# Kernel tuning notes

Hardware: AMD Instinct MI355X
Metric: run time of the kernel (lower is better)

The kernel has to match this reference:

```python
import jax, jax.numpy as jnp
import numpy as np

LAM = 0.5          # lambda_ in DyGCN
GROUPS = 4
EPS_GN = 1e-5
EPS_LN = 1e-5


def _group_norm(y, w, b):
    # y: [B, Ch, N, T]; GroupNorm over (channels-in-group, N, T)
    B, Ch, N, T = y.shape
    yr = y.reshape(B, GROUPS, Ch // GROUPS, N, T)
    mu = yr.mean(axis=(2, 3, 4), keepdims=True)
    var = yr.var(axis=(2, 3, 4), keepdims=True)
    yn = ((yr - mu) * jax.lax.rsqrt(var + EPS_GN)).reshape(B, Ch, N, T)
    return yn * w[None, :, None, None] + b[None, :, None, None]


def _gtu(X, w, b, pw, pb, qw, qb):
    # grouped conv2d, kernel (1,k), stride 1, VALID; out channels = 2*H
    xc = jax.lax.conv_general_dilated(
        X, w, window_strides=(1, 1), padding='VALID',
        feature_group_count=GROUPS,
        dimension_numbers=('NCHW', 'OIHW', 'NCHW'))
    xc = xc + b[None, :, None, None]
    H = X.shape[1]
    xp = _group_norm(xc[:, :H], pw, pb)   # matches torch chunk(2, dim=1)
    xq = _group_norm(xc[:, H:], qw, qb)
    mish = xp * jnp.tanh(jax.nn.softplus(xp))   # Mish
    gate = jnp.clip(xq, 0.0, 1.0)               # Hardtanh(0,1)
    return mish * gate


def reference(x, static_adj, U1, U2, U3, be, Ve, W0, b0, masks, Ws, bs, Wd, bd,
              conv3_w, conv5_w, conv7_w, conv9_w, conv_b,
              gn_pw, gn_pb, gn_qw, gn_qb, fc_w, fc_b, res_w, res_b, ln_w, ln_b):
    B, N, C, T = x.shape
    # ---- Temporal attention ----
    lhs = jnp.einsum('btc,cn->btn', jnp.einsum('bnct,n->btc', x, U1), U2)  # [B,T,N]
    rhs = jnp.einsum('c,bnct->bnt', U3, x)                                 # [B,N,T]
    product = jnp.einsum('btn,bns->bts', lhs, rhs)                          # [B,T,T]
    E = jnp.einsum('ij,bjk->bik', Ve, jax.nn.sigmoid(product + be))
    At = jax.nn.softmax(E, axis=1)
    x_TAt = jnp.einsum('bmt,bts->bms', x.reshape(B, N * C, T), At).reshape(B, N, C, T)
    # ---- DyGCN, vectorized across T ----
    xt = jnp.moveaxis(x_TAt, -1, 1)                                        # [B,T,N,C]
    x0 = jnp.einsum('btnc,hc->btnh', xt, W0) + b0                          # shared linear
    enh = static_adj[None] * jax.nn.sigmoid(masks)                         # [T,N,N]
    s = jnp.einsum('tnm,btmc->btnc', enh, xt)
    static_out = jnp.einsum('btnc,thc->btnh', s, Ws) + bs[None, :, None, :]
    # dynamic branch (DynamicGCNLayer): data-dependent adjacency
    scores = jnp.einsum('btnc,btmc->btnm', xt, xt) / jnp.sqrt(jnp.float32(C))
    adj = jax.nn.softmax(scores, axis=-1)                                  # [B,T,N,N]
    d = jnp.einsum('btnm,btmc->btnc', adj, xt)
    dyn_out = jnp.einsum('btnc,thc->btnh', d, Wd) + bd[None, :, None, :]
    fused = (LAM - 0.025) * static_out + (1.0 - LAM - 0.025) * dyn_out + 0.05 * x0
    X = jnp.transpose(fused, (0, 3, 2, 1))                                 # [B,H,N,T]
    # ---- multi-scale gated temporal convs ----
    outs = [
        _gtu(X, conv3_w, conv_b[0], gn_pw[0], gn_pb[0], gn_qw[0], gn_qb[0]),
        _gtu(X, conv5_w, conv_b[1], gn_pw[1], gn_pb[1], gn_qw[1], gn_qb[1]),
        _gtu(X, conv7_w, conv_b[2], gn_pw[2], gn_pb[2], gn_qw[2], gn_qb[2]),
        _gtu(X, conv9_w, conv_b[3], gn_pw[3], gn_pb[3], gn_qw[3], gn_qb[3]),
    ]
    tc = jnp.concatenate(outs, axis=-1)                                    # [B,H,N,4T-20]
    tc = jnp.einsum('bhnk,ok->bhno', tc, fc_w) + fc_b                      # fcmy (dropout=eval no-op)
    tco = jax.nn.relu(tc)                                                  # [B,H,N,T]
    # ---- residual + LayerNorm ----
    residual = jnp.einsum('bnct,hc->bhnt', x, res_w) + res_b[None, :, None, None]
    y = jax.nn.relu(residual + tco)                                        # [B,H,N,T]
    yp = jnp.transpose(y, (0, 3, 2, 1))                                    # [B,T,N,H]
    mu = yp.mean(axis=-1, keepdims=True)
    var = yp.var(axis=-1, keepdims=True)
    yn = (yp - mu) * jax.lax.rsqrt(var + EPS_LN) * ln_w + ln_b
    return jnp.transpose(yn, (0, 2, 3, 1))                                 # [B,N,H,T]


def setup_inputs():
    key = jax.random.key(0)
    ks = jax.random.split(key, 32)
    B, N, C, T, H = 16, 512, 64, 12, 64
    w = 0.05
    A = jax.random.uniform(ks[0], (N, N), jnp.float32)
    A = A / A.sum(axis=-1, keepdims=True)  # row-normalized static adjacency
    return {
        'x': jax.random.normal(ks[1], (B, N, C, T), jnp.float32),
        'static_adj': A,
        'U1': jax.random.normal(ks[2], (N,), jnp.float32) * w,
        'U2': jax.random.normal(ks[3], (C, N), jnp.float32) * w,
        'U3': jax.random.normal(ks[4], (C,), jnp.float32) * w,
        'be': jax.random.normal(ks[5], (1, T, T), jnp.float32) * w,
        'Ve': jax.random.normal(ks[6], (T, T), jnp.float32) * w,
        'W0': jax.random.normal(ks[7], (H, C), jnp.float32) * w,
        'b0': jnp.zeros((H,), jnp.float32),
        'masks': jax.random.uniform(ks[8], (T, N, N), jnp.float32, 0.8, 1.2),
        'Ws': jax.random.normal(ks[9], (T, H, C), jnp.float32) * w,
        'bs': jnp.zeros((T, H), jnp.float32),
        'Wd': jax.random.normal(ks[10], (T, H, C), jnp.float32) * w,
        'bd': jnp.zeros((T, H), jnp.float32),
        'conv3_w': jax.random.normal(ks[11], (2 * H, H // 4, 1, 3), jnp.float32) * w,
        'conv5_w': jax.random.normal(ks[12], (2 * H, H // 4, 1, 5), jnp.float32) * w,
        'conv7_w': jax.random.normal(ks[13], (2 * H, H // 4, 1, 7), jnp.float32) * w,
        'conv9_w': jax.random.normal(ks[14], (2 * H, H // 4, 1, 9), jnp.float32) * w,
        'conv_b': jnp.zeros((4, 2 * H), jnp.float32),
        'gn_pw': jnp.ones((4, H), jnp.float32),
        'gn_pb': jnp.zeros((4, H), jnp.float32),
        'gn_qw': jnp.ones((4, H), jnp.float32),
        'gn_qb': jnp.zeros((4, H), jnp.float32),
        'fc_w': jax.random.normal(ks[15], (T, 4 * T - 20), jnp.float32) * w,
        'fc_b': jnp.zeros((T,), jnp.float32),
        'res_w': jax.random.normal(ks[16], (H, C), jnp.float32) * w,
        'res_b': jnp.zeros((H,), jnp.float32),
        'ln_w': jnp.ones((H,), jnp.float32),
        'ln_b': jnp.zeros((H,), jnp.float32),
    }
```

## Files before the change

### kernel.cpp

```cpp
#include <hip/hip_runtime.h>

constexpr int Bb = 16, Nn = 512, Cc = 64, Tt = 12, Hh = 64;
constexpr int NCT = Nn * Cc * Tt;
constexpr int CT  = Cc * Tt;

__global__ void k0_rest(const float* __restrict__ rw, float* __restrict__ resT) {
    int i = blockIdx.x * 256 + threadIdx.x;
    if (i < Hh * Cc) {
        int h = i >> 6, c = i & 63;
        resT[c * 64 + h] = rw[i];
    }
}

__global__ void k1a_tmp1(const float* __restrict__ x, const float* __restrict__ U1,
                         float* __restrict__ tmp1) {
    int blk = blockIdx.x;
    int b = blk / 12; int r = blk % 12;
    int ctb = r >> 2; int nch = r & 3;
    int ct = ctb * 256 + threadIdx.x;
    const float* xb = x + (size_t)b * NCT;
    float acc = 0.f;
    int n0 = nch * 128;
    for (int n = n0; n < n0 + 128; ++n)
        acc += xb[n * CT + ct] * U1[n];
    atomicAdd(&tmp1[b * CT + ct], acc);
}

__global__ void k1b_rhs(const float* __restrict__ x, const float* __restrict__ U3,
                        float* __restrict__ rhs) {
    int wid = blockIdx.x * 4 + (threadIdx.x >> 6);
    int b = wid >> 9; int n = wid & 511;
    int l = threadIdx.x & 63;
    const float4* x4 = (const float4*)(x + (size_t)(b * Nn + n) * CT);
    float4 a0 = x4[3 * l], a1 = x4[3 * l + 1], a2 = x4[3 * l + 2];
    float xv[12] = {a0.x,a0.y,a0.z,a0.w, a1.x,a1.y,a1.z,a1.w, a2.x,a2.y,a2.z,a2.w};
    float u = U3[l];
    float p[12];
    #pragma unroll
    for (int t = 0; t < 12; ++t) p[t] = u * xv[t];
    #pragma unroll
    for (int off = 1; off < 64; off <<= 1) {
        #pragma unroll
        for (int t = 0; t < 12; ++t) p[t] += __shfl_xor(p[t], off);
    }
    if (l == 0) {
        float* rp = rhs + (size_t)(b * Nn + n) * 12;
        *(float4*)(rp)     = make_float4(p[0], p[1], p[2], p[3]);
        *(float4*)(rp + 4) = make_float4(p[4], p[5], p[6], p[7]);
        *(float4*)(rp + 8) = make_float4(p[8], p[9], p[10], p[11]);
    }
}

__global__ void k1c_att(const float* __restrict__ tmp1, const float* __restrict__ rhs,
                        const float* __restrict__ U2, const float* __restrict__ be,
                        const float* __restrict__ Ve, float* __restrict__ At) {
    __shared__ float t1[CT];
    __shared__ float rh[Nn * Tt];
    __shared__ float lh[Tt * Nn];
    __shared__ float part[576];
    __shared__ float sp[144];
    __shared__ float Ee[144];
    int b = blockIdx.x, tid = threadIdx.x;
    for (int i = tid; i < CT; i += 256) t1[i] = tmp1[b * CT + i];
    for (int i = tid; i < Nn * Tt; i += 256) rh[i] = rhs[b * Nn * Tt + i];
    __syncthreads();
    for (int nn = tid; nn < Nn; nn += 256) {
        float l[Tt];
        #pragma unroll
        for (int t = 0; t < Tt; ++t) l[t] = 0.f;
        for (int c = 0; c < Cc; ++c) {
            float u2 = U2[c * Nn + nn];
            #pragma unroll
            for (int t = 0; t < Tt; ++t) l[t] += t1[c * Tt + t] * u2;
        }
        #pragma unroll
        for (int t = 0; t < Tt; ++t) lh[t * Nn + nn] = l[t];
    }
    __syncthreads();
    for (int task = tid; task < 576; task += 256) {
        int ts = task >> 2, ch = task & 3;
        int t = ts / 12, s2 = ts % 12;
        int n0 = ch * 128;
        float a = 0.f;
        for (int nn = n0; nn < n0 + 128; ++nn) a += lh[t * Nn + nn] * rh[nn * Tt + s2];
        part[task] = a;
    }
    __syncthreads();
    if (tid < 144) {
        float a = part[tid * 4] + part[tid * 4 + 1] + part[tid * 4 + 2] + part[tid * 4 + 3]
                + be[tid];
        sp[tid] = 1.f / (1.f + __expf(-a));
    }
    __syncthreads();
    if (tid < 144) {
        int i = tid / 12, k = tid % 12;
        float a = 0.f;
        #pragma unroll
        for (int j = 0; j < 12; ++j) a += Ve[i * 12 + j] * sp[j * 12 + k];
        Ee[tid] = a;
    }
    __syncthreads();
    if (tid < 12) {
        int k = tid;
        float mx = -1e30f;
        #pragma unroll
        for (int i = 0; i < 12; ++i) mx = fmaxf(mx, Ee[i * 12 + k]);
        float su = 0.f; float ex[12];
        #pragma unroll
        for (int i = 0; i < 12; ++i) { ex[i] = __expf(Ee[i * 12 + k] - mx); su += ex[i]; }
        float inv = 1.f / su;
        #pragma unroll
        for (int i = 0; i < 12; ++i) At[b * 144 + i * 12 + k] = ex[i] * inv;
    }
}

__global__ void k2_xtt(const float* __restrict__ x, const float* __restrict__ At,
                       float* __restrict__ xtT) {
    int idx = blockIdx.x * 256 + threadIdx.x;
    int n = idx & 511; int c = (idx >> 9) & 63; int b = idx >> 15;
    const float* xr = x + (size_t)((b * Nn + n) * Cc + c) * Tt;
    float xv[Tt];
    {
        const float4* x4 = (const float4*)xr;
        float4 a0 = x4[0], a1 = x4[1], a2 = x4[2];
        xv[0]=a0.x; xv[1]=a0.y; xv[2]=a0.z; xv[3]=a0.w;
        xv[4]=a1.x; xv[5]=a1.y; xv[6]=a1.z; xv[7]=a1.w;
        xv[8]=a2.x; xv[9]=a2.y; xv[10]=a2.z; xv[11]=a2.w;
    }
    const float* Ab = At + b * 144;
    for (int t = 0; t < Tt; ++t) {
        float a = 0.f;
        #pragma unroll
        for (int u = 0; u < Tt; ++u) a += xv[u] * Ab[u * 12 + t];
        xtT[((size_t)(b * Tt + t) * Cc + c) * Nn + n] = a;
    }
}

__global__ void k2b_enh(const float* __restrict__ adj, const float* __restrict__ masks,
                        float* __restrict__ enhT) {
    __shared__ float tile[32][33];
    int blk = blockIdx.x;
    int t = blk >> 8; int r = blk & 255;
    int n0 = (r >> 4) * 32; int m0 = (r & 15) * 32;
    int tx = threadIdx.x & 31; int ty = threadIdx.x >> 5;
    #pragma unroll
    for (int i = 0; i < 4; ++i) {
        int nl = ty + 8 * i;
        float a  = adj[(n0 + nl) * Nn + m0 + tx];
        float mk = masks[t * Nn * Nn + (n0 + nl) * Nn + m0 + tx];
        tile[nl][tx] = a / (1.f + __expf(-mk));
    }
    __syncthreads();
    #pragma unroll
    for (int i = 0; i < 4; ++i) {
        int ml = ty + 8 * i;
        enhT[(size_t)(t * Nn + m0 + ml) * Nn + n0 + tx] = tile[tx][ml];
    }
}

__global__ __launch_bounds__(256, 3) void k3_gcn(
    const float* __restrict__ xtT, const float* __restrict__ enhT,
    const float* __restrict__ W0, const float* __restrict__ b0,
    const float* __restrict__ Ws, const float* __restrict__ bs,
    const float* __restrict__ Wd, const float* __restrict__ bd,
    float* __restrict__ F) {
    __shared__ float xs[64][64];
    int blk = blockIdx.x;
    int seg = blk & 7; int t = (blk >> 3) % Tt; int b = blk / (Tt * 8);
    int tid = threadIdx.x;
    int lane = tid & 63;
    int w = tid >> 6;
    int cg = lane >> 4;
    int r = lane & 15;
    int n = seg * 64 + w * 16 + r;
    int c0 = cg * 16;
    const float* xb = xtT + (size_t)(b * Tt + t) * Cc * Nn;
    float row[16], accd[16], accs[16];
    #pragma unroll
    for (int j = 0; j < 16; ++j) row[j] = xb[(c0 + j) * Nn + n];
    #pragma unroll
    for (int j = 0; j < 16; ++j) { accd[j] = 0.f; accs[j] = 0.f; }
    float sumexp = 0.f;
    const float* ehT = enhT + (size_t)t * Nn * Nn + n;
    for (int m0 = 0; m0 < Nn; m0 += 64) {
        __syncthreads();
        #pragma unroll
        for (int i = 0; i < 4; ++i) {
            int f = i * 256 + tid;
            int c = f >> 4; int mi = (f & 15) * 4;
            *(float4*)&xs[c][mi] = *(const float4*)(xb + c * Nn + m0 + mi);
        }
        __syncthreads();
        #pragma unroll 1
        for (int m4 = 0; m4 < 64; m4 += 4) {
            float e0 = ehT[(m0 + m4 + 0) * Nn];
            float e1 = ehT[(m0 + m4 + 1) * Nn];
            float e2 = ehT[(m0 + m4 + 2) * Nn];
            float e3 = ehT[(m0 + m4 + 3) * Nn];
            float4 v[16];
            #pragma unroll
            for (int j = 0; j < 16; ++j) v[j] = *(const float4*)&xs[c0 + j][m4];
            float s0 = 0.f, s1 = 0.f, s2 = 0.f, s3 = 0.f;
            #pragma unroll
            for (int j = 0; j < 16; ++j) {
                float rj = row[j];
                s0 += rj * v[j].x; s1 += rj * v[j].y;
                s2 += rj * v[j].z; s3 += rj * v[j].w;
            }
            s0 += __shfl_xor(s0, 16); s0 += __shfl_xor(s0, 32);
            s1 += __shfl_xor(s1, 16); s1 += __shfl_xor(s1, 32);
            s2 += __shfl_xor(s2, 16); s2 += __shfl_xor(s2, 32);
            s3 += __shfl_xor(s3, 16); s3 += __shfl_xor(s3, 32);
            float p0 = __expf(s0 * 0.125f), p1 = __expf(s1 * 0.125f);
            float p2 = __expf(s2 * 0.125f), p3 = __expf(s3 * 0.125f);
            sumexp += (p0 + p1) + (p2 + p3);
            #pragma unroll
            for (int j = 0; j < 16; ++j) {
                accd[j] += p0 * v[j].x + p1 * v[j].y + p2 * v[j].z + p3 * v[j].w;
                accs[j] += e0 * v[j].x + e1 * v[j].y + e2 * v[j].z + e3 * v[j].w;
            }
        }
    }
    float invd = 0.475f / sumexp;
    #pragma unroll
    for (int j = 0; j < 16; ++j) {
        accd[j] *= invd; accs[j] *= 0.475f; row[j] *= 0.05f;
    }
    const float* Wst = Ws + t * Hh * Cc;
    const float* Wdt = Wd + t * Hh * Cc;
    float* Fp = F + ((size_t)(b * Tt + t) * Nn + n) * Hh;
    for (int hb = 0; hb < 16; ++hb) {
        float oo[4];
        #pragma unroll
        for (int k = 0; k < 4; ++k) {
            int h = hb * 4 + k;
            const float4* w04 = (const float4*)(W0 + h * Cc + c0);
            const float4* ws4 = (const float4*)(Wst + h * Cc + c0);
            const float4* wd4 = (const float4*)(Wdt + h * Cc + c0);
            float a = 0.f;
            #pragma unroll
            for (int jj = 0; jj < 4; ++jj) {
                float4 wv = w04[jj], sv = ws4[jj], dv = wd4[jj];
                a += row[jj*4+0]*wv.x + row[jj*4+1]*wv.y + row[jj*4+2]*wv.z + row[jj*4+3]*wv.w;
                a += accs[jj*4+0]*sv.x + accs[jj*4+1]*sv.y + accs[jj*4+2]*sv.z + accs[jj*4+3]*sv.w;
                a += accd[jj*4+0]*dv.x + accd[jj*4+1]*dv.y + accd[jj*4+2]*dv.z + accd[jj*4+3]*dv.w;
            }
            a += __shfl_xor(a, 16);
            a += __shfl_xor(a, 32);
            oo[k] = a + 0.05f * b0[h] + 0.475f * (bs[t * Hh + h] + bd[t * Hh + h]);
        }
        if ((hb >> 2) == cg)
            *(float4*)(Fp + hb * 4) = make_float4(oo[0], oo[1], oo[2], oo[3]);
    }
}

__global__ __launch_bounds__(512) void k4_conv(
                        const float* __restrict__ F,
                        const float* __restrict__ w3, const float* __restrict__ w5,
                        const float* __restrict__ w7, const float* __restrict__ w9,
                        const float* __restrict__ cb,
                        float* __restrict__ xc, float* __restrict__ stats) {
    __shared__ float fl[4 * Tt * Hh];
    __shared__ float sstat[64];
    int blk = blockIdx.x;
    int b = blk >> 7; int n0 = (blk & 127) * 4;
    int tid = threadIdx.x;
    if (tid < 64) sstat[tid] = 0.f;
    for (int i = tid; i < 3072; i += 512) {
        int t = i >> 8; int r = i & 255;
        fl[i] = F[(size_t)(b * Tt + t) * Nn * Hh + n0 * Hh + r];
    }
    __syncthreads();
    int nl = tid >> 7; int co = tid & 127;
    int g = co >> 5;
    float a3[10], a5[8], a7[6], a9[4];
    {
        float c3 = cb[co], c5 = cb[128 + co], c7 = cb[256 + co], c9 = cb[384 + co];
        #pragma unroll
        for (int j = 0; j < 10; ++j) a3[j] = c3;
        #pragma unroll
        for (int j = 0; j < 8; ++j) a5[j] = c5;
        #pragma unroll
        for (int j = 0; j < 6; ++j) a7[j] = c7;
        #pragma unroll
        for (int j = 0; j < 4; ++j) a9[j] = c9;
    }
    for (int ci = 0; ci < 16; ++ci) {
        int cig = g * 16 + ci;
        float xr[12];
        #pragma unroll
        for (int tt = 0; tt < 12; ++tt) xr[tt] = fl[tt * 256 + nl * 64 + cig];
        const float* p3 = w3 + (co * 16 + ci) * 3;
        #pragma unroll
        for (int dt = 0; dt < 3; ++dt) {
            float wv = p3[dt];
            #pragma unroll
            for (int j = 0; j < 10; ++j) a3[j] += xr[j + dt] * wv;
        }
        const float* p5 = w5 + (co * 16 + ci) * 5;
        #pragma unroll
        for (int dt = 0; dt < 5; ++dt) {
            float wv = p5[dt];
            #pragma unroll
            for (int j = 0; j < 8; ++j) a5[j] += xr[j + dt] * wv;
        }
        const float* p7 = w7 + (co * 16 + ci) * 7;
        #pragma unroll
        for (int dt = 0; dt < 7; ++dt) {
            float wv = p7[dt];
            #pragma unroll
            for (int j = 0; j < 6; ++j) a7[j] += xr[j + dt] * wv;
        }
        const float* p9 = w9 + (co * 16 + ci) * 9;
        #pragma unroll
        for (int dt = 0; dt < 9; ++dt) {
            float wv = p9[dt];
            #pragma unroll
            for (int j = 0; j < 4; ++j) a9[j] += xr[j + dt] * wv;
        }
    }
    int pg = (co < 64) ? (co >> 4) : 4 + ((co - 64) >> 4);
    float* xcw = xc + ((size_t)(b * Nn + n0 + nl) * 128 + co) * 28;
    float su, sq;
    su = 0.f; sq = 0.f;
    #pragma unroll
    for (int j = 0; j < 10; ++j) { float v = a3[j]; xcw[j] = v; su += v; sq += v * v; }
    #pragma unroll
    for (int off = 1; off < 16; off <<= 1) { su += __shfl_xor(su, off); sq += __shfl_xor(sq, off); }
    if ((tid & 15) == 0) { atomicAdd(&sstat[(0 * 8 + pg) * 2], su); atomicAdd(&sstat[(0 * 8 + pg) * 2 + 1], sq); }
    su = 0.f; sq = 0.f;
    #pragma unroll
    for (int j = 0; j < 8; ++j) { float v = a5[j]; xcw[10 + j] = v; su += v; sq += v * v; }
    #pragma unroll
    for (int off = 1; off < 16; off <<= 1) { su += __shfl_xor(su, off); sq += __shfl_xor(sq, off); }
    if ((tid & 15) == 0) { atomicAdd(&sstat[(1 * 8 + pg) * 2], su); atomicAdd(&sstat[(1 * 8 + pg) * 2 + 1], sq); }
    su = 0.f; sq = 0.f;
    #pragma unroll
    for (int j = 0; j < 6; ++j) { float v = a7[j]; xcw[18 + j] = v; su += v; sq += v * v; }
    #pragma unroll
    for (int off = 1; off < 16; off <<= 1) { su += __shfl_xor(su, off); sq += __shfl_xor(sq, off); }
    if ((tid & 15) == 0) { atomicAdd(&sstat[(2 * 8 + pg) * 2], su); atomicAdd(&sstat[(2 * 8 + pg) * 2 + 1], sq); }
    su = 0.f; sq = 0.f;
    #pragma unroll
    for (int j = 0; j < 4; ++j) { float v = a9[j]; xcw[24 + j] = v; su += v; sq += v * v; }
    #pragma unroll
    for (int off = 1; off < 16; off <<= 1) { su += __shfl_xor(su, off); sq += __shfl_xor(sq, off); }
    if ((tid & 15) == 0) { atomicAdd(&sstat[(3 * 8 + pg) * 2], su); atomicAdd(&sstat[(3 * 8 + pg) * 2 + 1], sq); }
    __syncthreads();
    if (tid < 64) {
        int s = tid >> 4; int pgq = (tid >> 1) & 7; int st = tid & 1;
        atomicAdd(&stats[((s * Bb + b) * 8 + pgq) * 2 + st], sstat[(s * 8 + pgq) * 2 + st]);
    }
}

__global__ __launch_bounds__(256) void k5_final(
                         const float* __restrict__ xc, const float* __restrict__ stats,
                         const float* __restrict__ x,
                         const float* __restrict__ gpw, const float* __restrict__ gpb,
                         const float* __restrict__ gqw, const float* __restrict__ gqb,
                         const float* __restrict__ fcw, const float* __restrict__ fcb,
                         const float* __restrict__ resT, const float* __restrict__ rb,
                         const float* __restrict__ lnw, const float* __restrict__ lnb,
                         float* __restrict__ out) {
    int blk = blockIdx.x;
    int b = blk >> 7; int n = (blk & 127) * 4 + (threadIdx.x >> 6);
    int h = threadIdx.x & 63;
    int pg = h >> 4;
    const int TkA[4] = {10, 8, 6, 4};
    float mu_p[4], rs_p[4], mu_q[4], rs_q[4];
    #pragma unroll
    for (int s = 0; s < 4; ++s) {
        float cnt = 16.f * 512.f * (float)TkA[s];
        float su = stats[((s * Bb + b) * 8 + pg) * 2];
        float sq = stats[((s * Bb + b) * 8 + pg) * 2 + 1];
        float mu = su / cnt; float var = sq / cnt - mu * mu;
        mu_p[s] = mu; rs_p[s] = rsqrtf(var + 1e-5f);
        su = stats[((s * Bb + b) * 8 + 4 + pg) * 2];
        sq = stats[((s * Bb + b) * 8 + 4 + pg) * 2 + 1];
        mu = su / cnt; var = sq / cnt - mu * mu;
        mu_q[s] = mu; rs_q[s] = rsqrtf(var + 1e-5f);
    }
    const float* xcp = xc + ((size_t)(b * Nn + n) * 128 + h) * 28;
    const float* xcq = xcp + 64 * 28;
    float pb_[28], qb_[28];
    {
        const float4* p4 = (const float4*)xcp;
        const float4* q4 = (const float4*)xcq;
        #pragma unroll
        for (int j = 0; j < 7; ++j) {
            float4 a = p4[j];
            pb_[j*4] = a.x; pb_[j*4+1] = a.y; pb_[j*4+2] = a.z; pb_[j*4+3] = a.w;
            float4 c = q4[j];
            qb_[j*4] = c.x; qb_[j*4+1] = c.y; qb_[j*4+2] = c.z; qb_[j*4+3] = c.w;
        }
    }
    float tc[28];
    int off = 0;
    #pragma unroll
    for (int s = 0; s < 4; ++s) {
        float pw = gpw[s * 64 + h], pbv = gpb[s * 64 + h];
        float qw = gqw[s * 64 + h], qbv = gqb[s * 64 + h];
        #pragma unroll
        for (int j = 0; j < 10; ++j) {
            if (j < TkA[s]) {
                float p = (pb_[off + j] - mu_p[s]) * rs_p[s] * pw + pbv;
                float q = (qb_[off + j] - mu_q[s]) * rs_q[s] * qw + qbv;
                float mish;
                if (p > 20.f) mish = p;
                else { float z = 1.f + __expf(p); float z2 = z * z; mish = p * (z2 - 1.f) / (z2 + 1.f); }
                float gate = fminf(fmaxf(q, 0.f), 1.f);
                tc[off + j] = mish * gate;
            }
        }
        off += TkA[s];
    }
    float o[12];
    #pragma unroll
    for (int t = 0; t < 12; ++t) {
        float a = fcb[t];
        #pragma unroll
        for (int k = 0; k < 28; ++k) a += tc[k] * fcw[t * 28 + k];
        o[t] = fmaxf(a, 0.f);
    }
    const float* xr = x + (size_t)(b * Nn + n) * CT;
    float res[12];
    float rbv = rb[h];
    #pragma unroll
    for (int t = 0; t < 12; ++t) res[t] = rbv;
    for (int c = 0; c < 64; ++c) {
        float rv = resT[c * 64 + h];
        #pragma unroll
        for (int t = 0; t < 12; ++t) res[t] += xr[c * 12 + t] * rv;
    }
    float y[12];
    #pragma unroll
    for (int t = 0; t < 12; ++t) y[t] = fmaxf(res[t] + o[t], 0.f);
    float lw = lnw[h], lb = lnb[h];
    float ov[12];
    #pragma unroll
    for (int t = 0; t < 12; ++t) {
        float s1 = y[t], s2 = y[t] * y[t];
        #pragma unroll
        for (int o2 = 32; o2 > 0; o2 >>= 1) {
            s1 += __shfl_xor(s1, o2);
            s2 += __shfl_xor(s2, o2);
        }
        float mu = s1 * (1.f / 64.f);
        float var = s2 * (1.f / 64.f) - mu * mu;
        ov[t] = (y[t] - mu) * rsqrtf(var + 1e-5f) * lw + lb;
    }
    float* op = out + ((size_t)(b * Nn + n) * Hh + h) * Tt;
    *(float4*)(op)     = make_float4(ov[0], ov[1], ov[2], ov[3]);
    *(float4*)(op + 4) = make_float4(ov[4], ov[5], ov[6], ov[7]);
    *(float4*)(op + 8) = make_float4(ov[8], ov[9], ov[10], ov[11]);
}

extern "C" void kernel_launch(void* const* d_in, const int* in_sizes, int n_in,
                              void* d_out, int out_size, void* d_ws, size_t ws_size,
                              hipStream_t stream) {
    const float* x    = (const float*)d_in[0];
    const float* adj  = (const float*)d_in[1];
    const float* U1   = (const float*)d_in[2];
    const float* U2   = (const float*)d_in[3];
    const float* U3   = (const float*)d_in[4];
    const float* be   = (const float*)d_in[5];
    const float* Ve   = (const float*)d_in[6];
    const float* W0   = (const float*)d_in[7];
    const float* b0   = (const float*)d_in[8];
    const float* masks= (const float*)d_in[9];
    const float* Ws   = (const float*)d_in[10];
    const float* bs   = (const float*)d_in[11];
    const float* Wd   = (const float*)d_in[12];
    const float* bd   = (const float*)d_in[13];
    const float* w3   = (const float*)d_in[14];
    const float* w5   = (const float*)d_in[15];
    const float* w7   = (const float*)d_in[16];
    const float* w9   = (const float*)d_in[17];
    const float* cb   = (const float*)d_in[18];
    const float* gpw  = (const float*)d_in[19];
    const float* gpb  = (const float*)d_in[20];
    const float* gqw  = (const float*)d_in[21];
    const float* gqb  = (const float*)d_in[22];
    const float* fcw  = (const float*)d_in[23];
    const float* fcb  = (const float*)d_in[24];
    const float* rw   = (const float*)d_in[25];
    const float* rb   = (const float*)d_in[26];
    const float* lnw  = (const float*)d_in[27];
    const float* lnb  = (const float*)d_in[28];
    float* out = (float*)d_out;
    float* ws  = (float*)d_ws;

    float* tmp1  = ws;
    float* stats = ws + 12288;
    float* At    = ws + 13312;
    float* rhs   = ws + 15616;
    float* resT  = ws + 113920;
    float* xtT   = ws + 118016;
    float* enhT  = ws + 6409472;
    float* F     = ws + 9555200;
    float* xc    = ws + 15846656;

    hipMemsetAsync(ws, 0, 13312 * sizeof(float), stream);

    k0_rest<<<16, 256, 0, stream>>>(rw, resT);
    k1a_tmp1<<<192, 256, 0, stream>>>(x, U1, tmp1);
    k1b_rhs<<<2048, 256, 0, stream>>>(x, U3, rhs);
    k2b_enh<<<3072, 256, 0, stream>>>(adj, masks, enhT);
    k1c_att<<<16, 256, 0, stream>>>(tmp1, rhs, U2, be, Ve, At);
    k2_xtt<<<2048, 256, 0, stream>>>(x, At, xtT);
    k3_gcn<<<1536, 256, 0, stream>>>(xtT, enhT, W0, b0, Ws, bs, Wd, bd, F);
    k4_conv<<<2048, 512, 0, stream>>>(F, w3, w5, w7, w9, cb, xc, stats);
    k5_final<<<2048, 256, 0, stream>>>(xc, stats, x, gpw, gpb, gqw, gqb,
                                       fcw, fcb, resT, rb, lnw, lnb, out);
}
```

Baseline: 1.315 ms.

## Switch GCN input to node-major layout, widen per-thread channel tiles, split lhs kernel

Result: slower. 1.405 ms (+6.8%).

```diff
diff --git a/kernel.cpp b/kernel.cpp
--- a/kernel.cpp
+++ b/kernel.cpp
@@ -51,31 +51,35 @@
     }
 }
 
-__global__ void k1c_att(const float* __restrict__ tmp1, const float* __restrict__ rhs,
-                        const float* __restrict__ U2, const float* __restrict__ be,
-                        const float* __restrict__ Ve, float* __restrict__ At) {
+__global__ void k1c_lhs(const float* __restrict__ tmp1, const float* __restrict__ U2,
+                        float* __restrict__ lhG) {
     __shared__ float t1[CT];
+    int b = blockIdx.x >> 1; int nn = (blockIdx.x & 1) * 256 + threadIdx.x;
+    for (int i = threadIdx.x; i < CT; i += 256) t1[i] = tmp1[b * CT + i];
+    __syncthreads();
+    float l[Tt];
+    #pragma unroll
+    for (int t = 0; t < Tt; ++t) l[t] = 0.f;
+    for (int c = 0; c < Cc; ++c) {
+        float u2 = U2[c * Nn + nn];
+        #pragma unroll
+        for (int t = 0; t < Tt; ++t) l[t] += t1[c * Tt + t] * u2;
+    }
+    #pragma unroll
+    for (int t = 0; t < Tt; ++t) lhG[(size_t)(b * Tt + t) * Nn + nn] = l[t];
+}
+
+__global__ void k1c_att(const float* __restrict__ lhG, const float* __restrict__ rhs,
+                        const float* __restrict__ be, const float* __restrict__ Ve,
+                        float* __restrict__ At) {
     __shared__ float rh[Nn * Tt];
     __shared__ float lh[Tt * Nn];
     __shared__ float part[576];
     __shared__ float sp[144];
     __shared__ float Ee[144];
     int b = blockIdx.x, tid = threadIdx.x;
-    for (int i = tid; i < CT; i += 256) t1[i] = tmp1[b * CT + i];
     for (int i = tid; i < Nn * Tt; i += 256) rh[i] = rhs[b * Nn * Tt + i];
-    __syncthreads();
-    for (int nn = tid; nn < Nn; nn += 256) {
-        float l[Tt];
-        #pragma unroll
-        for (int t = 0; t < Tt; ++t) l[t] = 0.f;
-        for (int c = 0; c < Cc; ++c) {
-            float u2 = U2[c * Nn + nn];
-            #pragma unroll
-            for (int t = 0; t < Tt; ++t) l[t] += t1[c * Tt + t] * u2;
-        }
-        #pragma unroll
-        for (int t = 0; t < Tt; ++t) lh[t * Nn + nn] = l[t];
-    }
+    for (int i = tid; i < Tt * Nn; i += 256) lh[i] = lhG[(size_t)b * Tt * Nn + i];
     __syncthreads();
     for (int task = tid; task < 576; task += 256) {
         int ts = task >> 2, ch = task & 3;
@@ -115,24 +119,20 @@
 }
 
 __global__ void k2_xtt(const float* __restrict__ x, const float* __restrict__ At,
-                       float* __restrict__ xtT) {
+                       float* __restrict__ xtN) {
     int idx = blockIdx.x * 256 + threadIdx.x;
-    int n = idx & 511; int c = (idx >> 9) & 63; int b = idx >> 15;
-    const float* xr = x + (size_t)((b * Nn + n) * Cc + c) * Tt;
-    float xv[Tt];
-    {
-        const float4* x4 = (const float4*)xr;
-        float4 a0 = x4[0], a1 = x4[1], a2 = x4[2];
-        xv[0]=a0.x; xv[1]=a0.y; xv[2]=a0.z; xv[3]=a0.w;
-        xv[4]=a1.x; xv[5]=a1.y; xv[6]=a1.z; xv[7]=a1.w;
-        xv[8]=a2.x; xv[9]=a2.y; xv[10]=a2.z; xv[11]=a2.w;
-    }
+    int c = idx & 63; int n = (idx >> 6) & 511; int b = idx >> 15;
+    const float4* x4 = (const float4*)(x + (size_t)((b * Nn + n) * Cc + c) * Tt);
+    float4 a0 = x4[0], a1 = x4[1], a2 = x4[2];
+    float xv[12] = {a0.x,a0.y,a0.z,a0.w, a1.x,a1.y,a1.z,a1.w, a2.x,a2.y,a2.z,a2.w};
     const float* Ab = At + b * 144;
+    float* op = xtN + (size_t)b * Tt * Nn * Cc + n * Cc + c;
+    #pragma unroll
     for (int t = 0; t < Tt; ++t) {
         float a = 0.f;
         #pragma unroll
         for (int u = 0; u < Tt; ++u) a += xv[u] * Ab[u * 12 + t];
-        xtT[((size_t)(b * Tt + t) * Cc + c) * Nn + n] = a;
+        op[(size_t)t * Nn * Cc] = a;
     }
 }
 
@@ -158,72 +158,87 @@
     }
 }
 
-__global__ __launch_bounds__(256, 3) void k3_gcn(
-    const float* __restrict__ xtT, const float* __restrict__ enhT,
+__global__ __launch_bounds__(256) __attribute__((amdgpu_waves_per_eu(1, 3)))
+void k3_gcn(
+    const float* __restrict__ xtN, const float* __restrict__ enhT,
     const float* __restrict__ W0, const float* __restrict__ b0,
     const float* __restrict__ Ws, const float* __restrict__ bs,
     const float* __restrict__ Wd, const float* __restrict__ bd,
     float* __restrict__ F) {
     __shared__ float xs[64][64];
-    int blk = blockIdx.x;
-    int seg = blk & 7; int t = (blk >> 3) % Tt; int b = blk / (Tt * 8);
+    int blk = (blockIdx.x & 7) * 96 + (blockIdx.x >> 3);
+    int seg = blk & 3; int t = (blk >> 2) % Tt; int b = blk / 48;
     int tid = threadIdx.x;
     int lane = tid & 63;
     int w = tid >> 6;
-    int cg = lane >> 4;
-    int r = lane & 15;
-    int n = seg * 64 + w * 16 + r;
-    int c0 = cg * 16;
-    const float* xb = xtT + (size_t)(b * Tt + t) * Cc * Nn;
-    float row[16], accd[16], accs[16];
-    #pragma unroll
-    for (int j = 0; j < 16; ++j) row[j] = xb[(c0 + j) * Nn + n];
-    #pragma unroll
-    for (int j = 0; j < 16; ++j) { accd[j] = 0.f; accs[j] = 0.f; }
+    int half = lane >> 5;
+    int r = lane & 31;
+    int n = seg * 128 + w * 32 + r;
+    int c0 = half * 32;
+    const float* xb = xtN + (size_t)(b * Tt + t) * Nn * Cc;
+    float row[32];
+    {
+        const float4* r4 = (const float4*)(xb + n * Cc + c0);
+        #pragma unroll
+        for (int jj = 0; jj < 8; ++jj) {
+            float4 a = r4[jj];
+            row[jj*4] = a.x; row[jj*4+1] = a.y; row[jj*4+2] = a.z; row[jj*4+3] = a.w;
+        }
+    }
+    float accd[32], accs[32];
+    #pragma unroll
+    for (int j = 0; j < 32; ++j) { accd[j] = 0.f; accs[j] = 0.f; }
     float sumexp = 0.f;
-    const float* ehT = enhT + (size_t)t * Nn * Nn + n;
+    const float* eh = enhT + (size_t)t * Nn * Nn + n;
     for (int m0 = 0; m0 < Nn; m0 += 64) {
         __syncthreads();
-        #pragma unroll
-        for (int i = 0; i < 4; ++i) {
-            int f = i * 256 + tid;
-            int c = f >> 4; int mi = (f & 15) * 4;
-            *(float4*)&xs[c][mi] = *(const float4*)(xb + c * Nn + m0 + mi);
+        {
+            const float4* src = (const float4*)(xb + m0 * Cc);
+            float4* dst = (float4*)&xs[0][0];
+            #pragma unroll
+            for (int i = 0; i < 4; ++i) dst[i * 256 + tid] = src[i * 256 + tid];
         }
         __syncthreads();
         #pragma unroll 1
-        for (int m4 = 0; m4 < 64; m4 += 4) {
-            float e0 = ehT[(m0 + m4 + 0) * Nn];
-            float e1 = ehT[(m0 + m4 + 1) * Nn];
-            float e2 = ehT[(m0 + m4 + 2) * Nn];
-            float e3 = ehT[(m0 + m4 + 3) * Nn];
-            float4 v[16];
-            #pragma unroll
-            for (int j = 0; j < 16; ++j) v[j] = *(const float4*)&xs[c0 + j][m4];
-            float s0 = 0.f, s1 = 0.f, s2 = 0.f, s3 = 0.f;
-            #pragma unroll
-            for (int j = 0; j < 16; ++j) {
-                float rj = row[j];
-                s0 += rj * v[j].x; s1 += rj * v[j].y;
-                s2 += rj * v[j].z; s3 += rj * v[j].w;
-            }
-            s0 += __shfl_xor(s0, 16); s0 += __shfl_xor(s0, 32);
-            s1 += __shfl_xor(s1, 16); s1 += __shfl_xor(s1, 32);
-            s2 += __shfl_xor(s2, 16); s2 += __shfl_xor(s2, 32);
-            s3 += __shfl_xor(s3, 16); s3 += __shfl_xor(s3, 32);
-            float p0 = __expf(s0 * 0.125f), p1 = __expf(s1 * 0.125f);
-            float p2 = __expf(s2 * 0.125f), p3 = __expf(s3 * 0.125f);
-            sumexp += (p0 + p1) + (p2 + p3);
-            #pragma unroll
-            for (int j = 0; j < 16; ++j) {
-                accd[j] += p0 * v[j].x + p1 * v[j].y + p2 * v[j].z + p3 * v[j].w;
-                accs[j] += e0 * v[j].x + e1 * v[j].y + e2 * v[j].z + e3 * v[j].w;
-            }
+        for (int m = 0; m < 64; ++m) {
+            const float4* vp = (const float4*)&xs[m][c0];
+            float4 v0 = vp[0], v1 = vp[1], v2 = vp[2], v3 = vp[3];
+            float4 v4 = vp[4], v5 = vp[5], v6 = vp[6], v7 = vp[7];
+            float sa, sb;
+            sa = row[0]*v0.x + row[1]*v0.y + row[2]*v0.z + row[3]*v0.w
+               + row[4]*v1.x + row[5]*v1.y + row[6]*v1.z + row[7]*v1.w
+               + row[8]*v2.x + row[9]*v2.y + row[10]*v2.z + row[11]*v2.w
+               + row[12]*v3.x + row[13]*v3.y + row[14]*v3.z + row[15]*v3.w;
+            sb = row[16]*v4.x + row[17]*v4.y + row[18]*v4.z + row[19]*v4.w
+               + row[20]*v5.x + row[21]*v5.y + row[22]*v5.z + row[23]*v5.w
+               + row[24]*v6.x + row[25]*v6.y + row[26]*v6.z + row[27]*v6.w
+               + row[28]*v7.x + row[29]*v7.y + row[30]*v7.z + row[31]*v7.w;
+            float s = sa + sb;
+            s += __shfl_xor(s, 32);
+            float p = __expf(s * 0.125f);
+            sumexp += p;
+            float e = eh[(size_t)(m0 + m) * Nn];
+            accd[0]  += p*v0.x; accd[1]  += p*v0.y; accd[2]  += p*v0.z; accd[3]  += p*v0.w;
+            accd[4]  += p*v1.x; accd[5]  += p*v1.y; accd[6]  += p*v1.z; accd[7]  += p*v1.w;
+            accd[8]  += p*v2.x; accd[9]  += p*v2.y; accd[10] += p*v2.z; accd[11] += p*v2.w;
+            accd[12] += p*v3.x; accd[13] += p*v3.y; accd[14] += p*v3.z; accd[15] += p*v3.w;
+            accd[16] += p*v4.x; accd[17] += p*v4.y; accd[18] += p*v4.z; accd[19] += p*v4.w;
+            accd[20] += p*v5.x; accd[21] += p*v5.y; accd[22] += p*v5.z; accd[23] += p*v5.w;
+            accd[24] += p*v6.x; accd[25] += p*v6.y; accd[26] += p*v6.z; accd[27] += p*v6.w;
+            accd[28] += p*v7.x; accd[29] += p*v7.y; accd[30] += p*v7.z; accd[31] += p*v7.w;
+            accs[0]  += e*v0.x; accs[1]  += e*v0.y; accs[2]  += e*v0.z; accs[3]  += e*v0.w;
+            accs[4]  += e*v1.x; accs[5]  += e*v1.y; accs[6]  += e*v1.z; accs[7]  += e*v1.w;
+            accs[8]  += e*v2.x; accs[9]  += e*v2.y; accs[10] += e*v2.z; accs[11] += e*v2.w;
+            accs[12] += e*v3.x; accs[13] += e*v3.y; accs[14] += e*v3.z; accs[15] += e*v3.w;
+            accs[16] += e*v4.x; accs[17] += e*v4.y; accs[18] += e*v4.z; accs[19] += e*v4.w;
+            accs[20] += e*v5.x; accs[21] += e*v5.y; accs[22] += e*v5.z; accs[23] += e*v5.w;
+            accs[24] += e*v6.x; accs[25] += e*v6.y; accs[26] += e*v6.z; accs[27] += e*v6.w;
+            accs[28] += e*v7.x; accs[29] += e*v7.y; accs[30] += e*v7.z; accs[31] += e*v7.w;
         }
     }
     float invd = 0.475f / sumexp;
     #pragma unroll
-    for (int j = 0; j < 16; ++j) {
+    for (int j = 0; j < 32; ++j) {
         accd[j] *= invd; accs[j] *= 0.475f; row[j] *= 0.05f;
     }
     const float* Wst = Ws + t * Hh * Cc;
@@ -239,17 +254,16 @@
             const float4* wd4 = (const float4*)(Wdt + h * Cc + c0);
             float a = 0.f;
             #pragma unroll
-            for (int jj = 0; jj < 4; ++jj) {
+            for (int jj = 0; jj < 8; ++jj) {
                 float4 wv = w04[jj], sv = ws4[jj], dv = wd4[jj];
                 a += row[jj*4+0]*wv.x + row[jj*4+1]*wv.y + row[jj*4+2]*wv.z + row[jj*4+3]*wv.w;
                 a += accs[jj*4+0]*sv.x + accs[jj*4+1]*sv.y + accs[jj*4+2]*sv.z + accs[jj*4+3]*sv.w;
                 a += accd[jj*4+0]*dv.x + accd[jj*4+1]*dv.y + accd[jj*4+2]*dv.z + accd[jj*4+3]*dv.w;
             }
-            a += __shfl_xor(a, 16);
             a += __shfl_xor(a, 32);
             oo[k] = a + 0.05f * b0[h] + 0.475f * (bs[t * Hh + h] + bd[t * Hh + h]);
         }
-        if ((hb >> 2) == cg)
+        if ((hb >> 3) == half)
             *(float4*)(Fp + hb * 4) = make_float4(oo[0], oo[1], oo[2], oo[3]);
     }
 }
@@ -320,29 +334,29 @@
         }
     }
     int pg = (co < 64) ? (co >> 4) : 4 + ((co - 64) >> 4);
-    float* xcw = xc + ((size_t)(b * Nn + n0 + nl) * 128 + co) * 28;
+    float* xcw = xc + (size_t)(b * Nn + n0 + nl) * 28 * 128 + co;
     float su, sq;
     su = 0.f; sq = 0.f;
     #pragma unroll
-    for (int j = 0; j < 10; ++j) { float v = a3[j]; xcw[j] = v; su += v; sq += v * v; }
+    for (int j = 0; j < 10; ++j) { float v = a3[j]; xcw[j * 128] = v; su += v; sq += v * v; }
     #pragma unroll
     for (int off = 1; off < 16; off <<= 1) { su += __shfl_xor(su, off); sq += __shfl_xor(sq, off); }
     if ((tid & 15) == 0) { atomicAdd(&sstat[(0 * 8 + pg) * 2], su); atomicAdd(&sstat[(0 * 8 + pg) * 2 + 1], sq); }
     su = 0.f; sq = 0.f;
     #pragma unroll
-    for (int j = 0; j < 8; ++j) { float v = a5[j]; xcw[10 + j] = v; su += v; sq += v * v; }
+    for (int j = 0; j < 8; ++j) { float v = a5[j]; xcw[(10 + j) * 128] = v; su += v; sq += v * v; }
     #pragma unroll
     for (int off = 1; off < 16; off <<= 1) { su += __shfl_xor(su, off); sq += __shfl_xor(sq, off); }
     if ((tid & 15) == 0) { atomicAdd(&sstat[(1 * 8 + pg) * 2], su); atomicAdd(&sstat[(1 * 8 + pg) * 2 + 1], sq); }
     su = 0.f; sq = 0.f;
     #pragma unroll
-    for (int j = 0; j < 6; ++j) { float v = a7[j]; xcw[18 + j] = v; su += v; sq += v * v; }
+    for (int j = 0; j < 6; ++j) { float v = a7[j]; xcw[(18 + j) * 128] = v; su += v; sq += v * v; }
     #pragma unroll
     for (int off = 1; off < 16; off <<= 1) { su += __shfl_xor(su, off); sq += __shfl_xor(sq, off); }
     if ((tid & 15) == 0) { atomicAdd(&sstat[(2 * 8 + pg) * 2], su); atomicAdd(&sstat[(2 * 8 + pg) * 2 + 1], sq); }
     su = 0.f; sq = 0.f;
     #pragma unroll
-    for (int j = 0; j < 4; ++j) { float v = a9[j]; xcw[24 + j] = v; su += v; sq += v * v; }
+    for (int j = 0; j < 4; ++j) { float v = a9[j]; xcw[(24 + j) * 128] = v; su += v; sq += v * v; }
     #pragma unroll
     for (int off = 1; off < 16; off <<= 1) { su += __shfl_xor(su, off); sq += __shfl_xor(sq, off); }
     if ((tid & 15) == 0) { atomicAdd(&sstat[(3 * 8 + pg) * 2], su); atomicAdd(&sstat[(3 * 8 + pg) * 2 + 1], sq); }
@@ -380,19 +394,12 @@
         mu = su / cnt; var = sq / cnt - mu * mu;
         mu_q[s] = mu; rs_q[s] = rsqrtf(var + 1e-5f);
     }
-    const float* xcp = xc + ((size_t)(b * Nn + n) * 128 + h) * 28;
-    const float* xcq = xcp + 64 * 28;
+    const float* xcp = xc + (size_t)(b * Nn + n) * 28 * 128;
     float pb_[28], qb_[28];
-    {
-        const float4* p4 = (const float4*)xcp;
-        const float4* q4 = (const float4*)xcq;
-        #pragma unroll
-        for (int j = 0; j < 7; ++j) {
-            float4 a = p4[j];
-            pb_[j*4] = a.x; pb_[j*4+1] = a.y; pb_[j*4+2] = a.z; pb_[j*4+3] = a.w;
-            float4 c = q4[j];
-            qb_[j*4] = c.x; qb_[j*4+1] = c.y; qb_[j*4+2] = c.z; qb_[j*4+3] = c.w;
-        }
+    #pragma unroll
+    for (int k = 0; k < 28; ++k) {
+        pb_[k] = xcp[k * 128 + h];
+        qb_[k] = xcp[k * 128 + 64 + h];
     }
     float tc[28];
     int off = 0;
@@ -495,10 +502,11 @@
     float* At    = ws + 13312;
     float* rhs   = ws + 15616;
     float* resT  = ws + 113920;
-    float* xtT   = ws + 118016;
+    float* xtN   = ws + 118016;
     float* enhT  = ws + 6409472;
     float* F     = ws + 9555200;
     float* xc    = ws + 15846656;
+    float* lhG   = xtN;
 
     hipMemsetAsync(ws, 0, 13312 * sizeof(float), stream);
 
@@ -506,9 +514,10 @@
     k1a_tmp1<<<192, 256, 0, stream>>>(x, U1, tmp1);
     k1b_rhs<<<2048, 256, 0, stream>>>(x, U3, rhs);
     k2b_enh<<<3072, 256, 0, stream>>>(adj, masks, enhT);
-    k1c_att<<<16, 256, 0, stream>>>(tmp1, rhs, U2, be, Ve, At);
-    k2_xtt<<<2048, 256, 0, stream>>>(x, At, xtT);
-    k3_gcn<<<1536, 256, 0, stream>>>(xtT, enhT, W0, b0, Ws, bs, Wd, bd, F);
+    k1c_lhs<<<32, 256, 0, stream>>>(tmp1, U2, lhG);
+    k1c_att<<<16, 256, 0, stream>>>(lhG, rhs, be, Ve, At);
+    k2_xtt<<<2048, 256, 0, stream>>>(x, At, xtN);
+    k3_gcn<<<768, 256, 0, stream>>>(xtN, enhT, W0, b0, Ws, bs, Wd, bd, F);
     k4_conv<<<2048, 512, 0, stream>>>(F, w3, w5, w7, w9, cb, xc, stats);
     k5_final<<<2048, 256, 0, stream>>>(xc, stats, x, gpw, gpb, gqw, gqb,
                                        fcw, fcb, resT, rb, lnw, lnb, out);
```
